# Kernel optimization log

Measured on AMD Instinct MI355X. Metric: run time of the kernel, lower is better.

Reference implementation:

```python
import jax, jax.numpy as jnp
import numpy as np

N_NODES = 100000
N_EDGES = 1600000
D_IN = 128
D_HID = 128
D_OUT = 64


def setup_inputs() -> dict:
    key = jax.random.key(0)
    ks = jax.random.split(key, 8)
    x = jax.random.normal(ks[0], (N_NODES, D_IN), dtype=jnp.float32)
    edge_index = jax.random.randint(ks[1], (2, N_EDGES), 0, N_NODES, dtype=jnp.int64)
    s = 1.0 / np.sqrt(D_IN)
    W1l = jax.random.uniform(ks[2], (D_IN, D_HID), minval=-s, maxval=s, dtype=jnp.float32)
    W1r = jax.random.uniform(ks[3], (D_IN, D_HID), minval=-s, maxval=s, dtype=jnp.float32)
    b1 = jnp.zeros((D_HID,), dtype=jnp.float32)
    s2 = 1.0 / np.sqrt(D_HID)
    W2l = jax.random.uniform(ks[4], (D_HID, D_OUT), minval=-s2, maxval=s2, dtype=jnp.float32)
    W2r = jax.random.uniform(ks[5], (D_HID, D_OUT), minval=-s2, maxval=s2, dtype=jnp.float32)
    b2 = jnp.zeros((D_OUT,), dtype=jnp.float32)
    return {"x": x, "edge_index": edge_index, "drpt": 0,
            "W1l": W1l, "W1r": W1r, "b1": b1,
            "W2l": W2l, "W2r": W2r, "b2": b2}


def _mean_aggregate(x, src, dst, n_nodes):
    # gather source features along edges, scatter-mean to destinations
    gathered = x[src]                                   # [E, d]
    summed = jax.ops.segment_sum(gathered, dst, num_segments=n_nodes)  # [N, d]
    deg = jax.ops.segment_sum(jnp.ones((src.shape[0],), x.dtype), dst,
                              num_segments=n_nodes)     # [N]
    return summed / jnp.maximum(deg, 1.0)[:, None]


def _sage_conv(x, src, dst, Wl, Wr, b):
    # PyG SAGEConv (mean): out = agg @ Wl + b + x @ Wr
    agg = _mean_aggregate(x, src, dst, x.shape[0])
    return agg @ Wl + b + x @ Wr


def reference(x, edge_index, drpt, W1l, W1r, b1, W2l, W2r, b2):
    src, dst = edge_index[0], edge_index[1]
    h = _sage_conv(x, src, dst, W1l, W1r, b1)
    h = jax.nn.relu(h)
    # dropout is identity at inference (training=False)
    out = _sage_conv(h, src, dst, W2l, W2r, b2)
    return out
```

## Files before the change

kernel.cpp:

```cpp
#include <hip/hip_runtime.h>
#include <hip/hip_bf16.h>


#define N_NODES 100000
#define NGRP 6250
#define NBKT 391
#define ECHUNK 8192
#define BCAP 12288
#define NXB 12500
#define NWB 192

typedef __attribute__((ext_vector_type(8))) short short8v;
typedef __attribute__((ext_vector_type(4))) float f32x4;
typedef __attribute__((ext_vector_type(2))) uint u32x2;

__device__ inline ushort bf16_rne(float f) {
    union { float f; uint u; } c; c.f = f;
    uint u = c.u;
    return (ushort)((u + 0x7FFFu + ((u >> 16) & 1u)) >> 16);
}
__device__ inline float bf16_f(ushort h) {
    union { uint u; float f; } c; c.u = (uint)h << 16;
    return c.f;
}
__device__ inline unsigned char fp8_enc(float f) {
    union { float f; uint u; } c; c.f = f;
    uint u = c.u;
    uint s = (u >> 24) & 0x80u;
    uint a = u & 0x7FFFFFFFu;
    uint code;
    if (a >= 0x3C800000u) {
        uint r = a + 0x7FFFFu + ((a >> 20) & 1u);
        int e = (int)(r >> 23) - 120;
        uint mm = (r >> 20) & 7u;
        code = ((uint)e << 3) | mm;
        if (code > 0x7Eu) code = 0x7Eu;
    } else {
        code = (uint)(__uint_as_float(a) * 512.0f + 0.5f);
    }
    return (unsigned char)(s | code);
}

__device__ inline void gl_lds16(const void* g, void* l) {
    __builtin_amdgcn_global_load_lds(
        (const __attribute__((address_space(1))) uint*)g,
        (__attribute__((address_space(3))) uint*)l, 16, 0, 0);
}
__device__ inline uint lds_off(const void* p) {
    return (uint)(size_t)(const __attribute__((address_space(3))) char*)p;
}

__global__ __launch_bounds__(256) void k_prep(const float* __restrict__ x,
                                              const float* __restrict__ W1l,
                                              const float* __restrict__ W1r,
                                              const float* __restrict__ W2l,
                                              const float* __restrict__ W2r,
                                              const int* __restrict__ dst, int E,
                                              ushort* __restrict__ xh,
                                              unsigned char* __restrict__ xf8,
                                              ushort* __restrict__ BT1h,
                                              ushort* __restrict__ BT1l,
                                              ushort* __restrict__ BT2h,
                                              ushort* __restrict__ BT2l,
                                              int* __restrict__ bhist) {
    __shared__ int hsh[NBKT];
    const int b = blockIdx.x;
    if (b < NXB) {
        int i = (b * 256 + threadIdx.x) * 4;
        float4 v = *(const float4*)&x[i];
        ushort4 hh;
        hh.x = bf16_rne(v.x); hh.y = bf16_rne(v.y);
        hh.z = bf16_rne(v.z); hh.w = bf16_rne(v.w);
        *(ushort4*)&xh[i] = hh;
        uint f8 = (uint)fp8_enc(v.x) | ((uint)fp8_enc(v.y) << 8) |
                  ((uint)fp8_enc(v.z) << 16) | ((uint)fp8_enc(v.w) << 24);
        *(uint*)&xf8[i] = f8;
    } else if (b < NXB + NWB) {
        int id = (b - NXB) * 256 + threadIdx.x;
        if (id < 32768) {
            int n = id >> 8, k = id & 255;
            float v = (k < 128) ? W1l[k * 128 + n] : W1r[(k - 128) * 128 + n];
            ushort h = bf16_rne(v);
            BT1h[id] = h;
            BT1l[id] = bf16_rne(v - bf16_f(h));
        } else {
            int i = id - 32768;
            int n = i >> 7, k = i & 127;
            float v = (n < 64) ? W2l[k * 64 + n] : W2r[k * 64 + (n - 64)];
            ushort h = bf16_rne(v);
            BT2h[i] = h;
            BT2l[i] = bf16_rne(v - bf16_f(h));
        }
    } else {
        int bb = b - NXB - NWB;
        for (int i = threadIdx.x; i < NBKT; i += 256) hsh[i] = 0;
        __syncthreads();
        int b0 = bb * ECHUNK;
        for (int i = threadIdx.x; i < ECHUNK; i += 256) {
            int e = b0 + i;
            if (e < E) atomicAdd(&hsh[dst[e] >> 8], 1);
        }
        __syncthreads();
        for (int i = threadIdx.x; i < NBKT; i += 256)
            if (hsh[i]) atomicAdd(&bhist[i], hsh[i]);
    }
}

__global__ __launch_bounds__(512) void kA2_scan(const int* __restrict__ bhist,
                                                int* __restrict__ boff,
                                                int* __restrict__ bcur) {
    __shared__ int s[512];
    int t = threadIdx.x;
    s[t] = (t < NBKT) ? bhist[t] : 0;
    __syncthreads();
    for (int d = 1; d < 512; d <<= 1) {
        int v = (t >= d) ? s[t - d] : 0;
        __syncthreads();
        s[t] += v;
        __syncthreads();
    }
    if (t <= NBKT) {
        int e = (t == 0) ? 0 : s[t - 1];
        boff[t] = e;
        if (t < NBKT) bcur[t] = e;
    }
}

__global__ __launch_bounds__(256) void kA3_scatter(const int* __restrict__ src,
                                                   const int* __restrict__ dst,
                                                   int* __restrict__ bcur,
                                                   int* __restrict__ pairs, int E) {
    __shared__ int hist[NBKT];
    __shared__ int base[NBKT];
    __shared__ ushort rank[ECHUNK];
    for (int i = threadIdx.x; i < NBKT; i += 256) hist[i] = 0;
    __syncthreads();
    int b0 = blockIdx.x * ECHUNK;
    for (int i = threadIdx.x; i < ECHUNK; i += 256) {
        int e = b0 + i;
        if (e < E) rank[i] = (ushort)atomicAdd(&hist[dst[e] >> 8], 1);
    }
    __syncthreads();
    for (int i = threadIdx.x; i < NBKT; i += 256) {
        int c = hist[i];
        base[i] = c ? atomicAdd(&bcur[i], c) : 0;
    }
    __syncthreads();
    for (int i = threadIdx.x; i < ECHUNK; i += 256) {
        int e = b0 + i;
        if (e < E) {
            int d = dst[e];
            pairs[base[d >> 8] + rank[i]] = src[e] | ((d & 255) << 17);
        }
    }
}

__global__ __launch_bounds__(256) void kB_build(const int* __restrict__ pairs,
                                                const int* __restrict__ boff,
                                                int* __restrict__ csr,
                                                unsigned char* __restrict__ ldst,
                                                int* __restrict__ offsets,
                                                float* __restrict__ invdeg,
                                                int N, int E) {
    __shared__ int cnt[256];
    __shared__ int sc[256];
    __shared__ int cur[256];
    __shared__ int stage[BCAP];
    const int b = blockIdx.x;
    const int gbase = boff[b], gcount = boff[b + 1] - gbase;
    const int n0 = b << 8;
    const int t = threadIdx.x;

    cnt[t] = 0;
    __syncthreads();
    for (int i = t; i < gcount; i += 256)
        atomicAdd(&cnt[pairs[gbase + i] >> 17], 1);
    __syncthreads();
    sc[t] = cnt[t];
    __syncthreads();
    for (int d = 1; d < 256; d <<= 1) {
        int v = (t >= d) ? sc[t - d] : 0;
        __syncthreads();
        sc[t] += v;
        __syncthreads();
    }
    int excl = sc[t] - cnt[t];
    cur[t] = excl;
    int node = n0 + t;
    if (node < N) {
        offsets[node] = gbase + excl;
        invdeg[node] = 1.0f / fmaxf((float)cnt[t], 1.0f);
    }
    if (b == NBKT - 1 && t == 0) offsets[N] = E;
    __syncthreads();

    if (gcount <= BCAP) {
        for (int i = t; i < gcount; i += 256) {
            int p = pairs[gbase + i];
            int pos = atomicAdd(&cur[p >> 17], 1);
            stage[pos] = p;
        }
        __syncthreads();
        for (int i = t; i < gcount; i += 256) {
            int p = stage[i];
            csr[gbase + i] = p & 0x1FFFF;
            ldst[gbase + i] = (unsigned char)((p >> 17) & 15);
        }
    } else {
        for (int i = t; i < gcount; i += 256) {
            int p = pairs[gbase + i];
            int pos = atomicAdd(&cur[p >> 17], 1);
            csr[gbase + pos] = p & 0x1FFFF;
            ldst[gbase + pos] = (unsigned char)((p >> 17) & 15);
        }
    }
}

__global__ __launch_bounds__(256, 8) void k_agg1(const unsigned char* __restrict__ xf8,
                                                 const int* __restrict__ csr,
                                                 const unsigned char* __restrict__ ldst,
                                                 const int* __restrict__ off,
                                                 const float* __restrict__ invdeg,
                                                 ushort* __restrict__ ah, int E) {
    __shared__ char smem[16384];
    const int wv = threadIdx.x >> 6, lane = threadIdx.x & 63;
    const int g = blockIdx.x * 4 + wv;
    if (g >= NGRP) return;
    const int gbase = off[g * 16], gend = off[g * 16 + 16];
    const int cnt = gend - gbase;
    const int m = lane & 15;
    const int e_meta = lane & 31;
    const int t_hi = lane >> 5;
    const int Emax = E - 1;
    char* stg = smem + wv * 4096;

    f32x4 acc[8] = {};
    const int nch = (cnt + 31) >> 5;

    int pe = gbase + e_meta;
    int se = csr[(pe < Emax) ? pe : Emax];
    int lb = (pe < gend) ? (int)ldst[pe] : 255;

    for (int ch = 0; ch < nch; ++ch) {
        const char* rowbase = (const char*)xf8 + (size_t)se * 128;
        #pragma unroll
        for (int c = 0; c < 4; ++c)
            gl_lds16(rowbase + (c * 2 + t_hi) * 16, stg + c * 1024);

        int p = gbase + (ch + 1) * 32 + e_meta;
        se = csr[(p < Emax) ? p : Emax];
        int lbn = (p < gend) ? (int)ldst[p] : 255;

        asm volatile("s_waitcnt vmcnt(0)" ::: "memory");
        __builtin_amdgcn_sched_barrier(0);

        unsigned long long av = 0ull;
        #pragma unroll
        for (int j = 0; j < 8; ++j) {
            int k = (lane >> 4) * 8 + j;
            int b = __shfl(lb, k);
            av |= (b == m) ? (0x38ull << (8 * j)) : 0ull;
        }

        uint base0 = lds_off(stg) + lane * 8;
        #pragma unroll
        for (int th = 0; th < 2; ++th) {
            u32x2 tb[4];
            #pragma unroll
            for (int t = 0; t < 4; ++t) {
                uint a1 = base0 + (th * 4 + t) * 512;
                asm volatile("ds_read_b64_tr_b8 %0, %1" : "=v"(tb[t]) : "v"(a1));
            }
            asm volatile("s_waitcnt lgkmcnt(0)" ::: "memory");
            __builtin_amdgcn_sched_barrier(0);
            #pragma unroll
            for (int t = 0; t < 4; ++t) {
                unsigned long long bv = ((unsigned long long)tb[t].y << 32) | tb[t].x;
                acc[th * 4 + t] = __builtin_amdgcn_mfma_f32_16x16x32_fp8_fp8(
                    (long long)av, (long long)bv, acc[th * 4 + t], 0, 0, 0);
            }
            __builtin_amdgcn_sched_barrier(0);
        }
        lb = lbn;
    }

    float idv[4];
    #pragma unroll
    for (int i = 0; i < 4; ++i) idv[i] = invdeg[g * 16 + (lane >> 4) * 4 + i];
    #pragma unroll
    for (int t = 0; t < 8; ++t) {
        #pragma unroll
        for (int i = 0; i < 4; ++i) {
            int node = g * 16 + (lane >> 4) * 4 + i;
            ah[(size_t)node * 128 + t * 16 + m] = bf16_rne(acc[t][i] * idv[i]);
        }
    }
}

__global__ __launch_bounds__(256, 8) void k_agg2(const ushort* __restrict__ hWl,
                                                 const float* __restrict__ hWr,
                                                 const int* __restrict__ csr,
                                                 const unsigned char* __restrict__ ldst,
                                                 const int* __restrict__ off,
                                                 const float* __restrict__ invdeg,
                                                 const float* __restrict__ b2,
                                                 float* __restrict__ out, int E) {
    __shared__ char smem[16384];
    const int wv = threadIdx.x >> 6, lane = threadIdx.x & 63;
    const int g = blockIdx.x * 4 + wv;
    if (g >= NGRP) return;
    const int gbase = off[g * 16], gend = off[g * 16 + 16];
    const int cnt = gend - gbase;
    const int m = lane & 15;
    const int phys = lane >> 3;
    const int E4 = (phys < 4) ? phys * 2 : (phys - 4) * 2 + 1;
    const int e_st = E4 * 4 + ((lane >> 1) & 3);
    const int e_meta = lane & 31;
    const int Emax = E - 1;
    char* stg = smem + wv * 4096;

    f32x4 acc[4] = {};
    const int nch = (cnt + 31) >> 5;

    int ps = gbase + e_st;
    int se = csr[(ps < Emax) ? ps : Emax];
    int pm = gbase + e_meta;
    int lb = (pm < gend) ? (int)ldst[pm] : 255;

    for (int ch = 0; ch < nch; ++ch) {
        const char* gsrc = (const char*)hWl + (size_t)se * 128 + (lane & 1) * 16;
        #pragma unroll
        for (int c = 0; c < 4; ++c)
            gl_lds16(gsrc + c * 32, stg + c * 1024);

        int p = gbase + (ch + 1) * 32;
        int ps2 = p + e_st;
        se = csr[(ps2 < Emax) ? ps2 : Emax];
        int pm2 = p + e_meta;
        int lbn = (pm2 < gend) ? (int)ldst[pm2] : 255;

        asm volatile("s_waitcnt vmcnt(0)" ::: "memory");
        __builtin_amdgcn_sched_barrier(0);

        uint au[4];
        #pragma unroll
        for (int jp = 0; jp < 4; ++jp) {
            int k0 = (lane >> 4) * 8 + jp * 2;
            int b0 = __shfl(lb, k0);
            int b1 = __shfl(lb, k0 + 1);
            au[jp] = ((b0 == m) ? 0x3F80u : 0u) | (((b1 == m) ? 0x3F80u : 0u) << 16);
        }
        union { uint u[4]; short8v v; } A_;
        A_.u[0] = au[0]; A_.u[1] = au[1]; A_.u[2] = au[2]; A_.u[3] = au[3];

        uint base0 = lds_off(stg) + lane * 8;
        #pragma unroll
        for (int th = 0; th < 2; ++th) {
            u32x2 t1[2], t2[2];
            #pragma unroll
            for (int t = 0; t < 2; ++t) {
                uint a1 = base0 + (th * 2 + t) * 1024;
                uint a2 = a1 + 512;
                asm volatile("ds_read_b64_tr_b16 %0, %1" : "=v"(t1[t]) : "v"(a1));
                asm volatile("ds_read_b64_tr_b16 %0, %1" : "=v"(t2[t]) : "v"(a2));
            }
            asm volatile("s_waitcnt lgkmcnt(0)" ::: "memory");
            __builtin_amdgcn_sched_barrier(0);
            #pragma unroll
            for (int t = 0; t < 2; ++t) {
                union { uint u[4]; short8v v; } B_;
                B_.u[0] = t1[t].x; B_.u[1] = t1[t].y;
                B_.u[2] = t2[t].x; B_.u[3] = t2[t].y;
                acc[th * 2 + t] = __builtin_amdgcn_mfma_f32_16x16x32_bf16(
                    A_.v, B_.v, acc[th * 2 + t], 0, 0, 0);
            }
            __builtin_amdgcn_sched_barrier(0);
        }
        lb = lbn;
    }

    float idv[4];
    #pragma unroll
    for (int i = 0; i < 4; ++i) idv[i] = invdeg[g * 16 + (lane >> 4) * 4 + i];
    #pragma unroll
    for (int t = 0; t < 4; ++t) {
        #pragma unroll
        for (int i = 0; i < 4; ++i) {
            int node = g * 16 + (lane >> 4) * 4 + i;
            size_t idx = (size_t)node * 64 + t * 16 + m;
            out[idx] = acc[t][i] * idv[i] + hWr[idx] + b2[t * 16 + m];
        }
    }
}

__global__ __launch_bounds__(256) void k_mfma12(
    const ushort* __restrict__ Agg, const ushort* __restrict__ X,
    const ushort* __restrict__ B1h, const ushort* __restrict__ B1l,
    const ushort* __restrict__ B2h, const ushort* __restrict__ B2l,
    const float* __restrict__ b1,
    ushort* __restrict__ hWl, float* __restrict__ hWr, int M) {
    __shared__ ushort Ah[128 * 40], Bh[128 * 40], Bl[128 * 40];
    __shared__ ushort hT[4 * 128 * 40];

    const int tid = threadIdx.x;
    const int wid = tid >> 6, lane = tid & 63;
    const int wm = wid >> 1, wn = wid & 1;
    const int m0 = blockIdx.x * 128;
    const int rl = lane & 15, kof = (lane >> 4) * 8;
    const int rq = lane >> 4;

    f32x4 acc[4][4] = {};
    for (int kc = 0; kc < 8; ++kc) {
        #pragma unroll
        for (int r = 0; r < 2; ++r) {
            int chunk = tid + 256 * r;
            int row = chunk >> 2, cq = chunk & 3;
            int gk = kc * 32 + cq * 8;
            int ldso = row * 40 + cq * 8;
            int grow = m0 + row;
            if (grow >= M) grow = M - 1;
            if (gk >= 128) {
                *(short8v*)&Ah[ldso] = *(const short8v*)&X[(size_t)grow * 128 + gk - 128];
            } else {
                *(short8v*)&Ah[ldso] = *(const short8v*)&Agg[(size_t)grow * 128 + gk];
            }
            *(short8v*)&Bh[ldso] = *(const short8v*)&B1h[row * 256 + gk];
            *(short8v*)&Bl[ldso] = *(const short8v*)&B1l[row * 256 + gk];
        }
        __syncthreads();

        short8v a_h[4], b_h[4], b_l[4];
        #pragma unroll
        for (int f = 0; f < 4; ++f) {
            int ra = wm * 64 + f * 16 + rl;
            int rb = wn * 64 + f * 16 + rl;
            a_h[f] = *(const short8v*)&Ah[ra * 40 + kof];
            b_h[f] = *(const short8v*)&Bh[rb * 40 + kof];
            b_l[f] = *(const short8v*)&Bl[rb * 40 + kof];
        }
        #pragma unroll
        for (int mf = 0; mf < 4; ++mf)
            #pragma unroll
            for (int nf = 0; nf < 4; ++nf) {
                acc[mf][nf] = __builtin_amdgcn_mfma_f32_16x16x32_bf16(a_h[mf], b_h[nf], acc[mf][nf], 0, 0, 0);
                acc[mf][nf] = __builtin_amdgcn_mfma_f32_16x16x32_bf16(a_h[mf], b_l[nf], acc[mf][nf], 0, 0, 0);
            }
        __syncthreads();
    }

    #pragma unroll
    for (int mf = 0; mf < 4; ++mf)
        #pragma unroll
        for (int nf = 0; nf < 4; ++nf) {
            int col = wn * 64 + nf * 16 + rl;
            float bv = b1[col];
            #pragma unroll
            for (int i = 0; i < 4; ++i) {
                int rloc = wm * 64 + mf * 16 + rq * 4 + i;
                float v = fmaxf(acc[mf][nf][i] + bv, 0.0f);
                hT[((col >> 5) * 128 + rloc) * 40 + (col & 31)] = bf16_rne(v);
            }
        }
    __syncthreads();

    f32x4 acc2[4][4] = {};
    for (int kc = 0; kc < 4; ++kc) {
        #pragma unroll
        for (int r = 0; r < 2; ++r) {
            int chunk = tid + 256 * r;
            int row = chunk >> 2, cq = chunk & 3;
            int gk = kc * 32 + cq * 8;
            int ldso = row * 40 + cq * 8;
            *(short8v*)&Bh[ldso] = *(const short8v*)&B2h[row * 128 + gk];
            *(short8v*)&Bl[ldso] = *(const short8v*)&B2l[row * 128 + gk];
        }
        __syncthreads();

        short8v a_h[4], b_h[4], b_l[4];
        #pragma unroll
        for (int f = 0; f < 4; ++f) {
            int ra = wm * 64 + f * 16 + rl;
            int rb = wn * 64 + f * 16 + rl;
            a_h[f] = *(const short8v*)&hT[(kc * 128 + ra) * 40 + kof];
            b_h[f] = *(const short8v*)&Bh[rb * 40 + kof];
            b_l[f] = *(const short8v*)&Bl[rb * 40 + kof];
        }
        #pragma unroll
        for (int mf = 0; mf < 4; ++mf)
            #pragma unroll
            for (int nf = 0; nf < 4; ++nf) {
                acc2[mf][nf] = __builtin_amdgcn_mfma_f32_16x16x32_bf16(a_h[mf], b_h[nf], acc2[mf][nf], 0, 0, 0);
                acc2[mf][nf] = __builtin_amdgcn_mfma_f32_16x16x32_bf16(a_h[mf], b_l[nf], acc2[mf][nf], 0, 0, 0);
            }
        __syncthreads();
    }

    #pragma unroll
    for (int mf = 0; mf < 4; ++mf)
        #pragma unroll
        for (int nf = 0; nf < 4; ++nf) {
            int col = wn * 64 + nf * 16 + rl;
            #pragma unroll
            for (int i = 0; i < 4; ++i) {
                int row = m0 + wm * 64 + mf * 16 + rq * 4 + i;
                if (row < M) {
                    float v = acc2[mf][nf][i];
                    if (col < 64) hWl[(size_t)row * 64 + col] = bf16_rne(v);
                    else          hWr[(size_t)row * 64 + col - 64] = v;
                }
            }
        }
}

extern "C" void kernel_launch(void* const* d_in, const int* in_sizes, int n_in,
                              void* d_out, int out_size, void* d_ws, size_t ws_size,
                              hipStream_t stream) {
    const float* x   = (const float*)d_in[0];
    const int*   ei  = (const int*)d_in[1];
    const float* W1l = (const float*)d_in[3];
    const float* W1r = (const float*)d_in[4];
    const float* b1  = (const float*)d_in[5];
    const float* W2l = (const float*)d_in[6];
    const float* W2r = (const float*)d_in[7];
    const float* b2  = (const float*)d_in[8];
    float* out = (float*)d_out;

    const int N = N_NODES;
    const int E = in_sizes[1] / 2;
    const int* src = ei;
    const int* dst = ei + E;
    const int NEB = (E + ECHUNK - 1) / ECHUNK;

    char* ws = (char*)d_ws;
    int*           bhist   = (int*)   (ws + 0);
    int*           boff    = (int*)   (ws + 4096);
    int*           bcur    = (int*)   (ws + 8192);
    int*           offsets = (int*)   (ws + 12288);
    float*         invdeg  = (float*) (ws + 417792);
    int*           csr     = (int*)   (ws + 819200);
    unsigned char* ldst    = (unsigned char*)(ws + 7220224);
    unsigned char* x_f8    = (unsigned char*)(ws + 8821760);
    ushort*        x_hi    = (ushort*)(ws + 21622784);
    ushort*        agg_hi  = (ushort*)(ws + 47223808);
    float*         hWr     = (float*) (ws + 98425856);
    ushort*        BT1h    = (ushort*)(ws + 124026880);
    ushort*        BT1l    = (ushort*)(ws + 124092416);
    ushort*        BT2h    = (ushort*)(ws + 124157952);
    ushort*        BT2l    = (ushort*)(ws + 124190720);
    int*           pairs   = (int*)   (ws + 98425856);
    ushort*        hWl     = (ushort*)(ws + 72824832);

    hipMemsetAsync(bhist, 0, NBKT * 4, stream);

    k_prep<<<NXB + NWB + NEB, 256, 0, stream>>>(x, W1l, W1r, W2l, W2r, dst, E,
                                                x_hi, x_f8, BT1h, BT1l, BT2h, BT2l, bhist);
    kA2_scan<<<1, 512, 0, stream>>>(bhist, boff, bcur);
    kA3_scatter<<<NEB, 256, 0, stream>>>(src, dst, bcur, pairs, E);
    kB_build<<<NBKT, 256, 0, stream>>>(pairs, boff, csr, ldst, offsets, invdeg, N, E);

    const int GAGG = (NGRP + 3) / 4;
    k_agg1<<<GAGG, 256, 0, stream>>>(x_f8, csr, ldst, offsets, invdeg, agg_hi, E);

    const int MB = (N + 127) / 128;
    k_mfma12<<<MB, 256, 0, stream>>>(agg_hi, x_hi, BT1h, BT1l, BT2h, BT2l,
                                     b1, hWl, hWr, N);

    k_agg2<<<GAGG, 256, 0, stream>>>(hWl, hWr, csr, ldst, offsets, invdeg, b2, out, E);
}
```

Before: 198.2 us.

## Double-buffer gather staging in aggregation kernels and register-prefetch GEMM tiles

After: 199.5 us. About the same (+0.7%).

```diff
diff --git a/kernel.cpp b/kernel.cpp
--- a/kernel.cpp
+++ b/kernel.cpp
@@ -216,13 +216,13 @@
     }
 }
 
-__global__ __launch_bounds__(256, 8) void k_agg1(const unsigned char* __restrict__ xf8,
+__global__ __launch_bounds__(256, 5) void k_agg1(const unsigned char* __restrict__ xf8,
                                                  const int* __restrict__ csr,
                                                  const unsigned char* __restrict__ ldst,
                                                  const int* __restrict__ off,
                                                  const float* __restrict__ invdeg,
                                                  ushort* __restrict__ ah, int E) {
-    __shared__ char smem[16384];
+    __shared__ char smem[32768];
     const int wv = threadIdx.x >> 6, lane = threadIdx.x & 63;
     const int g = blockIdx.x * 4 + wv;
     if (g >= NGRP) return;
@@ -232,37 +232,53 @@
     const int e_meta = lane & 31;
     const int t_hi = lane >> 5;
     const int Emax = E - 1;
-    char* stg = smem + wv * 4096;
+    char* stg0 = smem + wv * 8192;
+    char* stg1 = stg0 + 4096;
 
     f32x4 acc[8] = {};
     const int nch = (cnt + 31) >> 5;
 
-    int pe = gbase + e_meta;
-    int se = csr[(pe < Emax) ? pe : Emax];
-    int lb = (pe < gend) ? (int)ldst[pe] : 255;
+    int p0 = gbase + e_meta;
+    int se_cur = csr[(p0 < Emax) ? p0 : Emax];
+    int lb_cur = (p0 < gend) ? (int)ldst[p0] : 255;
+    int p1 = p0 + 32;
+    int se_nxt = csr[(p1 < Emax) ? p1 : Emax];
+    int lb_nxt = (p1 < gend) ? (int)ldst[p1] : 255;
+
+    {
+        const char* rb = (const char*)xf8 + (size_t)se_cur * 128;
+        #pragma unroll
+        for (int c = 0; c < 4; ++c)
+            gl_lds16(rb + (c * 2 + t_hi) * 16, stg0 + c * 1024);
+    }
 
     for (int ch = 0; ch < nch; ++ch) {
-        const char* rowbase = (const char*)xf8 + (size_t)se * 128;
-        #pragma unroll
-        for (int c = 0; c < 4; ++c)
-            gl_lds16(rowbase + (c * 2 + t_hi) * 16, stg + c * 1024);
-
-        int p = gbase + (ch + 1) * 32 + e_meta;
-        se = csr[(p < Emax) ? p : Emax];
-        int lbn = (p < gend) ? (int)ldst[p] : 255;
-
-        asm volatile("s_waitcnt vmcnt(0)" ::: "memory");
+        char* curb = (ch & 1) ? stg1 : stg0;
+        char* nxtb = (ch & 1) ? stg0 : stg1;
+        int p2 = gbase + (ch + 2) * 32 + e_meta;
+        int se2 = csr[(p2 < Emax) ? p2 : Emax];
+        int lb2 = (p2 < gend) ? (int)ldst[p2] : 255;
+        __builtin_amdgcn_sched_barrier(0);
+        if (ch + 1 < nch) {
+            const char* rb = (const char*)xf8 + (size_t)se_nxt * 128;
+            #pragma unroll
+            for (int c = 0; c < 4; ++c)
+                gl_lds16(rb + (c * 2 + t_hi) * 16, nxtb + c * 1024);
+            asm volatile("s_waitcnt vmcnt(6)" ::: "memory");
+        } else {
+            asm volatile("s_waitcnt vmcnt(2)" ::: "memory");
+        }
         __builtin_amdgcn_sched_barrier(0);
 
         unsigned long long av = 0ull;
         #pragma unroll
         for (int j = 0; j < 8; ++j) {
             int k = (lane >> 4) * 8 + j;
-            int b = __shfl(lb, k);
+            int b = __shfl(lb_cur, k);
             av |= (b == m) ? (0x38ull << (8 * j)) : 0ull;
         }
 
-        uint base0 = lds_off(stg) + lane * 8;
+        uint base0 = lds_off(curb) + lane * 8;
         #pragma unroll
         for (int th = 0; th < 2; ++th) {
             u32x2 tb[4];
@@ -281,7 +297,7 @@
             }
             __builtin_amdgcn_sched_barrier(0);
         }
-        lb = lbn;
+        se_nxt = se2; lb_cur = lb_nxt; lb_nxt = lb2;
     }
 
     float idv[4];
@@ -297,7 +313,7 @@
     }
 }
 
-__global__ __launch_bounds__(256, 8) void k_agg2(const ushort* __restrict__ hWl,
+__global__ __launch_bounds__(256, 5) void k_agg2(const ushort* __restrict__ hWl,
                                                  const float* __restrict__ hWr,
                                                  const int* __restrict__ csr,
                                                  const unsigned char* __restrict__ ldst,
@@ -305,7 +321,7 @@
                                                  const float* __restrict__ invdeg,
                                                  const float* __restrict__ b2,
                                                  float* __restrict__ out, int E) {
-    __shared__ char smem[16384];
+    __shared__ char smem[32768];
     const int wv = threadIdx.x >> 6, lane = threadIdx.x & 63;
     const int g = blockIdx.x * 4 + wv;
     if (g >= NGRP) return;
@@ -317,43 +333,60 @@
     const int e_st = E4 * 4 + ((lane >> 1) & 3);
     const int e_meta = lane & 31;
     const int Emax = E - 1;
-    char* stg = smem + wv * 4096;
+    char* stg0 = smem + wv * 8192;
+    char* stg1 = stg0 + 4096;
 
     f32x4 acc[4] = {};
     const int nch = (cnt + 31) >> 5;
 
-    int ps = gbase + e_st;
-    int se = csr[(ps < Emax) ? ps : Emax];
-    int pm = gbase + e_meta;
-    int lb = (pm < gend) ? (int)ldst[pm] : 255;
+    int ps0 = gbase + e_st;
+    int se_cur = csr[(ps0 < Emax) ? ps0 : Emax];
+    int pm0 = gbase + e_meta;
+    int lb_cur = (pm0 < gend) ? (int)ldst[pm0] : 255;
+    int ps1 = ps0 + 32;
+    int se_nxt = csr[(ps1 < Emax) ? ps1 : Emax];
+    int pm1 = pm0 + 32;
+    int lb_nxt = (pm1 < gend) ? (int)ldst[pm1] : 255;
+
+    {
+        const char* gsrc = (const char*)hWl + (size_t)se_cur * 128 + (lane & 1) * 16;
+        #pragma unroll
+        for (int c = 0; c < 4; ++c)
+            gl_lds16(gsrc + c * 32, stg0 + c * 1024);
+    }
 
     for (int ch = 0; ch < nch; ++ch) {
-        const char* gsrc = (const char*)hWl + (size_t)se * 128 + (lane & 1) * 16;
-        #pragma unroll
-        for (int c = 0; c < 4; ++c)
-            gl_lds16(gsrc + c * 32, stg + c * 1024);
-
-        int p = gbase + (ch + 1) * 32;
-        int ps2 = p + e_st;
-        se = csr[(ps2 < Emax) ? ps2 : Emax];
-        int pm2 = p + e_meta;
-        int lbn = (pm2 < gend) ? (int)ldst[pm2] : 255;
-
-        asm volatile("s_waitcnt vmcnt(0)" ::: "memory");
+        char* curb = (ch & 1) ? stg1 : stg0;
+        char* nxtb = (ch & 1) ? stg0 : stg1;
+        int p2 = gbase + (ch + 2) * 32;
+        int p2s = p2 + e_st;
+        int se2 = csr[(p2s < Emax) ? p2s : Emax];
+        int p2m = p2 + e_meta;
+        int lb2 = (p2m < gend) ? (int)ldst[p2m] : 255;
+        __builtin_amdgcn_sched_barrier(0);
+        if (ch + 1 < nch) {
+            const char* gsrc = (const char*)hWl + (size_t)se_nxt * 128 + (lane & 1) * 16;
+            #pragma unroll
+            for (int c = 0; c < 4; ++c)
+                gl_lds16(gsrc + c * 32, nxtb + c * 1024);
+            asm volatile("s_waitcnt vmcnt(6)" ::: "memory");
+        } else {
+            asm volatile("s_waitcnt vmcnt(2)" ::: "memory");
+        }
         __builtin_amdgcn_sched_barrier(0);
 
         uint au[4];
         #pragma unroll
         for (int jp = 0; jp < 4; ++jp) {
             int k0 = (lane >> 4) * 8 + jp * 2;
-            int b0 = __shfl(lb, k0);
-            int b1 = __shfl(lb, k0 + 1);
+            int b0 = __shfl(lb_cur, k0);
+            int b1 = __shfl(lb_cur, k0 + 1);
             au[jp] = ((b0 == m) ? 0x3F80u : 0u) | (((b1 == m) ? 0x3F80u : 0u) << 16);
         }
         union { uint u[4]; short8v v; } A_;
         A_.u[0] = au[0]; A_.u[1] = au[1]; A_.u[2] = au[2]; A_.u[3] = au[3];
 
-        uint base0 = lds_off(stg) + lane * 8;
+        uint base0 = lds_off(curb) + lane * 8;
         #pragma unroll
         for (int th = 0; th < 2; ++th) {
             u32x2 t1[2], t2[2];
@@ -376,7 +409,7 @@
             }
             __builtin_amdgcn_sched_barrier(0);
         }
-        lb = lbn;
+        se_nxt = se2; lb_cur = lb_nxt; lb_nxt = lb2;
     }
 
     float idv[4];
@@ -409,25 +442,43 @@
     const int rl = lane & 15, kof = (lane >> 4) * 8;
     const int rq = lane >> 4;
 
+    const int r0 = tid >> 2, r1 = (tid + 256) >> 2;
+    const int cq = tid & 3;
+    int g0 = m0 + r0; if (g0 >= M) g0 = M - 1;
+    int g1 = m0 + r1; if (g1 >= M) g1 = M - 1;
+    const int ldso0 = r0 * 40 + cq * 8;
+    const int ldso1 = r1 * 40 + cq * 8;
+
+    short8v pA0, pA1, pB0, pB1, pL0, pL1;
+    {
+        int gk = cq * 8;
+        pA0 = *(const short8v*)&Agg[(size_t)g0 * 128 + gk];
+        pA1 = *(const short8v*)&Agg[(size_t)g1 * 128 + gk];
+        pB0 = *(const short8v*)&B1h[r0 * 256 + gk];
+        pB1 = *(const short8v*)&B1h[r1 * 256 + gk];
+        pL0 = *(const short8v*)&B1l[r0 * 256 + gk];
+        pL1 = *(const short8v*)&B1l[r1 * 256 + gk];
+    }
     f32x4 acc[4][4] = {};
     for (int kc = 0; kc < 8; ++kc) {
-        #pragma unroll
-        for (int r = 0; r < 2; ++r) {
-            int chunk = tid + 256 * r;
-            int row = chunk >> 2, cq = chunk & 3;
-            int gk = kc * 32 + cq * 8;
-            int ldso = row * 40 + cq * 8;
-            int grow = m0 + row;
-            if (grow >= M) grow = M - 1;
-            if (gk >= 128) {
-                *(short8v*)&Ah[ldso] = *(const short8v*)&X[(size_t)grow * 128 + gk - 128];
-            } else {
-                *(short8v*)&Ah[ldso] = *(const short8v*)&Agg[(size_t)grow * 128 + gk];
-            }
-            *(short8v*)&Bh[ldso] = *(const short8v*)&B1h[row * 256 + gk];
-            *(short8v*)&Bl[ldso] = *(const short8v*)&B1l[row * 256 + gk];
-        }
-        __syncthreads();
+        *(short8v*)&Ah[ldso0] = pA0; *(short8v*)&Ah[ldso1] = pA1;
+        *(short8v*)&Bh[ldso0] = pB0; *(short8v*)&Bh[ldso1] = pB1;
+        *(short8v*)&Bl[ldso0] = pL0; *(short8v*)&Bl[ldso1] = pL1;
+        __syncthreads();
+
+        if (kc < 7) {
+            int gk = (kc + 1) * 32 + cq * 8;
+            const ushort* s0 = (gk >= 128) ? &X[(size_t)g0 * 128 + gk - 128]
+                                           : &Agg[(size_t)g0 * 128 + gk];
+            const ushort* s1 = (gk >= 128) ? &X[(size_t)g1 * 128 + gk - 128]
+                                           : &Agg[(size_t)g1 * 128 + gk];
+            pA0 = *(const short8v*)s0;
+            pA1 = *(const short8v*)s1;
+            pB0 = *(const short8v*)&B1h[r0 * 256 + gk];
+            pB1 = *(const short8v*)&B1h[r1 * 256 + gk];
+            pL0 = *(const short8v*)&B1l[r0 * 256 + gk];
+            pL1 = *(const short8v*)&B1l[r1 * 256 + gk];
+        }
 
         short8v a_h[4], b_h[4], b_l[4];
         #pragma unroll
@@ -448,6 +499,15 @@
         __syncthreads();
     }
 
+    short8v qB0, qB1, qL0, qL1;
+    {
+        int gk = cq * 8;
+        qB0 = *(const short8v*)&B2h[r0 * 128 + gk];
+        qB1 = *(const short8v*)&B2h[r1 * 128 + gk];
+        qL0 = *(const short8v*)&B2l[r0 * 128 + gk];
+        qL1 = *(const short8v*)&B2l[r1 * 128 + gk];
+    }
+
     #pragma unroll
     for (int mf = 0; mf < 4; ++mf)
         #pragma unroll
@@ -465,16 +525,17 @@
 
     f32x4 acc2[4][4] = {};
     for (int kc = 0; kc < 4; ++kc) {
-        #pragma unroll
-        for (int r = 0; r < 2; ++r) {
-            int chunk = tid + 256 * r;
-            int row = chunk >> 2, cq = chunk & 3;
-            int gk = kc * 32 + cq * 8;
-            int ldso = row * 40 + cq * 8;
-            *(short8v*)&Bh[ldso] = *(const short8v*)&B2h[row * 128 + gk];
-            *(short8v*)&Bl[ldso] = *(const short8v*)&B2l[row * 128 + gk];
-        }
-        __syncthreads();
+        *(short8v*)&Bh[ldso0] = qB0; *(short8v*)&Bh[ldso1] = qB1;
+        *(short8v*)&Bl[ldso0] = qL0; *(short8v*)&Bl[ldso1] = qL1;
+        __syncthreads();
+
+        if (kc < 3) {
+            int gk = (kc + 1) * 32 + cq * 8;
+            qB0 = *(const short8v*)&B2h[r0 * 128 + gk];
+            qB1 = *(const short8v*)&B2h[r1 * 128 + gk];
+            qL0 = *(const short8v*)&B2l[r0 * 128 + gk];
+            qL1 = *(const short8v*)&B2l[r1 * 128 + gk];
+        }
 
         short8v a_h[4], b_h[4], b_l[4];
         #pragma unroll
```

## Prefetch next GEMM tiles into registers and sort CSR edges by source range

Applied to the files above, without the earlier changes.

Result: no change. 195.8 us (-1.2%).

```diff
diff --git a/kernel.cpp b/kernel.cpp
--- a/kernel.cpp
+++ b/kernel.cpp
@@ -162,34 +162,40 @@
                                                 int* __restrict__ offsets,
                                                 float* __restrict__ invdeg,
                                                 int N, int E) {
-    __shared__ int cnt[256];
-    __shared__ int sc[256];
+    __shared__ int cntk[256];
+    __shared__ int sck[256];
     __shared__ int cur[256];
+    __shared__ int cntn[256];
     __shared__ int stage[BCAP];
     const int b = blockIdx.x;
     const int gbase = boff[b], gcount = boff[b + 1] - gbase;
     const int n0 = b << 8;
     const int t = threadIdx.x;
 
-    cnt[t] = 0;
-    __syncthreads();
-    for (int i = t; i < gcount; i += 256)
-        atomicAdd(&cnt[pairs[gbase + i] >> 17], 1);
-    __syncthreads();
-    sc[t] = cnt[t];
+    cntk[t] = 0; cntn[t] = 0;
+    __syncthreads();
+    for (int i = t; i < gcount; i += 256) {
+        int p = pairs[gbase + i];
+        int dlow = (p >> 17) & 255;
+        int key = (dlow & 0xF0) | ((p & 0x1FFFF) >> 13);
+        atomicAdd(&cntk[key], 1);
+        atomicAdd(&cntn[dlow], 1);
+    }
+    __syncthreads();
+    sck[t] = cntk[t];
     __syncthreads();
     for (int d = 1; d < 256; d <<= 1) {
-        int v = (t >= d) ? sc[t - d] : 0;
-        __syncthreads();
-        sc[t] += v;
-        __syncthreads();
-    }
-    int excl = sc[t] - cnt[t];
-    cur[t] = excl;
+        int v = (t >= d) ? sck[t - d] : 0;
+        __syncthreads();
+        sck[t] += v;
+        __syncthreads();
+    }
+    cur[t] = sck[t] - cntk[t];
     int node = n0 + t;
     if (node < N) {
-        offsets[node] = gbase + excl;
-        invdeg[node] = 1.0f / fmaxf((float)cnt[t], 1.0f);
+        int gk = t & 0xF0;
+        offsets[node] = gbase + sck[gk] - cntk[gk];
+        invdeg[node] = 1.0f / fmaxf((float)cntn[t], 1.0f);
     }
     if (b == NBKT - 1 && t == 0) offsets[N] = E;
     __syncthreads();
@@ -197,7 +203,8 @@
     if (gcount <= BCAP) {
         for (int i = t; i < gcount; i += 256) {
             int p = pairs[gbase + i];
-            int pos = atomicAdd(&cur[p >> 17], 1);
+            int key = ((p >> 17) & 0xF0) | ((p & 0x1FFFF) >> 13);
+            int pos = atomicAdd(&cur[key], 1);
             stage[pos] = p;
         }
         __syncthreads();
@@ -209,7 +216,8 @@
     } else {
         for (int i = t; i < gcount; i += 256) {
             int p = pairs[gbase + i];
-            int pos = atomicAdd(&cur[p >> 17], 1);
+            int key = ((p >> 17) & 0xF0) | ((p & 0x1FFFF) >> 13);
+            int pos = atomicAdd(&cur[key], 1);
             csr[gbase + pos] = p & 0x1FFFF;
             ldst[gbase + pos] = (unsigned char)((p >> 17) & 15);
         }
@@ -409,25 +417,43 @@
     const int rl = lane & 15, kof = (lane >> 4) * 8;
     const int rq = lane >> 4;
 
+    const int r0 = tid >> 2, r1 = (tid + 256) >> 2;
+    const int cq = tid & 3;
+    int g0 = m0 + r0; if (g0 >= M) g0 = M - 1;
+    int g1 = m0 + r1; if (g1 >= M) g1 = M - 1;
+    const int ldso0 = r0 * 40 + cq * 8;
+    const int ldso1 = r1 * 40 + cq * 8;
+
+    short8v pA0, pA1, pB0, pB1, pL0, pL1;
+    {
+        int gk = cq * 8;
+        pA0 = *(const short8v*)&Agg[(size_t)g0 * 128 + gk];
+        pA1 = *(const short8v*)&Agg[(size_t)g1 * 128 + gk];
+        pB0 = *(const short8v*)&B1h[r0 * 256 + gk];
+        pB1 = *(const short8v*)&B1h[r1 * 256 + gk];
+        pL0 = *(const short8v*)&B1l[r0 * 256 + gk];
+        pL1 = *(const short8v*)&B1l[r1 * 256 + gk];
+    }
     f32x4 acc[4][4] = {};
     for (int kc = 0; kc < 8; ++kc) {
-        #pragma unroll
-        for (int r = 0; r < 2; ++r) {
-            int chunk = tid + 256 * r;
-            int row = chunk >> 2, cq = chunk & 3;
-            int gk = kc * 32 + cq * 8;
-            int ldso = row * 40 + cq * 8;
-            int grow = m0 + row;
-            if (grow >= M) grow = M - 1;
-            if (gk >= 128) {
-                *(short8v*)&Ah[ldso] = *(const short8v*)&X[(size_t)grow * 128 + gk - 128];
-            } else {
-                *(short8v*)&Ah[ldso] = *(const short8v*)&Agg[(size_t)grow * 128 + gk];
-            }
-            *(short8v*)&Bh[ldso] = *(const short8v*)&B1h[row * 256 + gk];
-            *(short8v*)&Bl[ldso] = *(const short8v*)&B1l[row * 256 + gk];
-        }
-        __syncthreads();
+        *(short8v*)&Ah[ldso0] = pA0; *(short8v*)&Ah[ldso1] = pA1;
+        *(short8v*)&Bh[ldso0] = pB0; *(short8v*)&Bh[ldso1] = pB1;
+        *(short8v*)&Bl[ldso0] = pL0; *(short8v*)&Bl[ldso1] = pL1;
+        __syncthreads();
+
+        if (kc < 7) {
+            int gk = (kc + 1) * 32 + cq * 8;
+            const ushort* s0 = (gk >= 128) ? &X[(size_t)g0 * 128 + gk - 128]
+                                           : &Agg[(size_t)g0 * 128 + gk];
+            const ushort* s1 = (gk >= 128) ? &X[(size_t)g1 * 128 + gk - 128]
+                                           : &Agg[(size_t)g1 * 128 + gk];
+            pA0 = *(const short8v*)s0;
+            pA1 = *(const short8v*)s1;
+            pB0 = *(const short8v*)&B1h[r0 * 256 + gk];
+            pB1 = *(const short8v*)&B1h[r1 * 256 + gk];
+            pL0 = *(const short8v*)&B1l[r0 * 256 + gk];
+            pL1 = *(const short8v*)&B1l[r1 * 256 + gk];
+        }
 
         short8v a_h[4], b_h[4], b_l[4];
         #pragma unroll
@@ -448,6 +474,15 @@
         __syncthreads();
     }
 
+    short8v qB0, qB1, qL0, qL1;
+    {
+        int gk = cq * 8;
+        qB0 = *(const short8v*)&B2h[r0 * 128 + gk];
+        qB1 = *(const short8v*)&B2h[r1 * 128 + gk];
+        qL0 = *(const short8v*)&B2l[r0 * 128 + gk];
+        qL1 = *(const short8v*)&B2l[r1 * 128 + gk];
+    }
+
     #pragma unroll
     for (int mf = 0; mf < 4; ++mf)
         #pragma unroll
@@ -465,16 +500,17 @@
 
     f32x4 acc2[4][4] = {};
     for (int kc = 0; kc < 4; ++kc) {
-        #pragma unroll
-        for (int r = 0; r < 2; ++r) {
-            int chunk = tid + 256 * r;
-            int row = chunk >> 2, cq = chunk & 3;
-            int gk = kc * 32 + cq * 8;
-            int ldso = row * 40 + cq * 8;
-            *(short8v*)&Bh[ldso] = *(const short8v*)&B2h[row * 128 + gk];
-            *(short8v*)&Bl[ldso] = *(const short8v*)&B2l[row * 128 + gk];
-        }
-        __syncthreads();
+        *(short8v*)&Bh[ldso0] = qB0; *(short8v*)&Bh[ldso1] = qB1;
+        *(short8v*)&Bl[ldso0] = qL0; *(short8v*)&Bl[ldso1] = qL1;
+        __syncthreads();
+
+        if (kc < 3) {
+            int gk = (kc + 1) * 32 + cq * 8;
+            qB0 = *(const short8v*)&B2h[r0 * 128 + gk];
+            qB1 = *(const short8v*)&B2h[r1 * 128 + gk];
+            qL0 = *(const short8v*)&B2l[r0 * 128 + gk];
+            qL1 = *(const short8v*)&B2l[r1 * 128 + gk];
+        }
 
         short8v a_h[4], b_h[4], b_l[4];
         #pragma unroll
```
